# Optimization experiments

Hardware: AMD Instinct MI355X
Metric: run time of the kernel (lower is better)

The kernel has to match this reference:

```python
import jax, jax.numpy as jnp
import numpy as np

N, B, D, H, E = 1024, 8, 768, 8, 16384
DH = D // H
EPS = 1e-5


def setup_inputs() -> dict:
    key = jax.random.key(0)
    ks = jax.random.split(key, 12)
    s = 0.02
    return {
        "x": jax.random.normal(ks[0], (N, B, D), jnp.float32),
        "edge_index": jax.random.randint(ks[1], (B, 2, E), 0, N, jnp.int32),
        "gcn_W": jax.random.normal(ks[2], (D, D), jnp.float32) * s,
        "gcn_b": jnp.zeros((D,), jnp.float32),
        "in_proj_w": jax.random.normal(ks[3], (3 * D, D), jnp.float32) * s,
        "in_proj_b": jnp.zeros((3 * D,), jnp.float32),
        "out_proj_w": jax.random.normal(ks[4], (D, D), jnp.float32) * s,
        "out_proj_b": jnp.zeros((D,), jnp.float32),
        "gate_w": jax.random.normal(ks[5], (D, 2 * D), jnp.float32) * s,
        "gate_b": jnp.zeros((D,), jnp.float32),
        "ln_g": jnp.ones((D,), jnp.float32),
        "ln_b": jnp.zeros((D,), jnp.float32),
    }


def _gcn(xb, edge_index, gcn_W, gcn_b):
    # xb: [B, N, D] node features; edge_index: [B, 2, E]
    h = xb @ gcn_W.T  # linear first, as in PyG GCNConv
    loops = jnp.arange(N, dtype=edge_index.dtype)

    def agg(h_b, ei_b):
        src = jnp.concatenate([ei_b[0], loops])  # add self-loops
        dst = jnp.concatenate([ei_b[1], loops])
        deg = jax.ops.segment_sum(jnp.ones_like(src, h_b.dtype), dst, num_segments=N)
        dinv = jnp.where(deg > 0, jax.lax.rsqrt(deg), 0.0)
        norm = dinv[src] * dinv[dst]  # symmetric normalization
        msg = norm[:, None] * h_b[src]
        return jax.ops.segment_sum(msg, dst, num_segments=N)

    return jax.vmap(agg)(h, edge_index) + gcn_b  # [B, N, D]


def _mha(x, in_proj_w, in_proj_b, out_proj_w, out_proj_b):
    # x: [N, B, D] (seq-first, as nn.MultiheadAttention default)
    qkv = x @ in_proj_w.T + in_proj_b  # [N, B, 3D]
    q, k, v = jnp.split(qkv, 3, axis=-1)

    def heads(t):  # [N, B, D] -> [B, H, N, DH]
        return t.reshape(N, B, H, DH).transpose(1, 2, 0, 3)

    q, k, v = heads(q), heads(k), heads(v)
    scores = jnp.einsum("bhqd,bhkd->bhqk", q, k) / jnp.sqrt(jnp.float32(DH))
    attn = jax.nn.softmax(scores, axis=-1)
    ctx = jnp.einsum("bhqk,bhkd->bhqd", attn, v)  # [B, H, N, DH]
    ctx = ctx.transpose(2, 0, 1, 3).reshape(N, B, D)
    return ctx @ out_proj_w.T + out_proj_b


def _layernorm(x, g, b):
    mu = jnp.mean(x, axis=-1, keepdims=True)
    var = jnp.mean(jnp.square(x - mu), axis=-1, keepdims=True)
    return (x - mu) * jax.lax.rsqrt(var + EPS) * g + b


def reference(x, edge_index, gcn_W, gcn_b, in_proj_w, in_proj_b,
              out_proj_w, out_proj_b, gate_w, gate_b, ln_g, ln_b):
    xb = x.transpose(1, 0, 2)  # [B, N, D]
    gcn_out = _gcn(xb, edge_index, gcn_W, gcn_b).transpose(1, 0, 2)  # [N, B, D]
    attn_out = _mha(x, in_proj_w, in_proj_b, out_proj_w, out_proj_b)  # [N, B, D]
    combined = jnp.concatenate([gcn_out, attn_out], axis=-1)
    gate = jax.nn.sigmoid(combined @ gate_w.T + gate_b)
    fused = gate * gcn_out + (1.0 - gate) * attn_out
    return _layernorm(fused + x, ln_g, ln_b)
```

## Files before the change

### kernel.cpp

```cpp
#include <hip/hip_runtime.h>


typedef __attribute__((ext_vector_type(8))) short b16x8;
typedef __attribute__((ext_vector_type(4))) float f32x4;

using gu32 = __attribute__((address_space(1))) const unsigned int;
using lu32 = __attribute__((address_space(3))) unsigned int;

constexpr int N  = 1024;
constexpr int B  = 8;
constexpr int D  = 768;
constexpr int H  = 8;
constexpr int DH = 96;
constexpr int E  = 16384;
constexpr int M  = N * B;
constexpr float LN_EPS = 1e-5f;

#define DEV static __device__ __forceinline__
#define GLOAD(SRC, DST) __builtin_amdgcn_global_load_lds((gu32*)(SRC), (lu32*)(DST), 16, 0, 0)

DEV unsigned short f2b(float f) {
  unsigned u = __float_as_uint(f);
  u += 0x7fffu + ((u >> 16) & 1u);
  return (unsigned short)(u >> 16);
}
DEV float b2f(unsigned short h) { return __uint_as_float(((unsigned)h) << 16); }

constexpr int CS0 = 1572864;
constexpr int CS1 = CS0 + 147456;
constexpr int CS2 = CS1 + 442368;
constexpr int CS3 = CS2 + 147456;
constexpr int CS4 = CS3 + 294912;
__global__ void cast_all_kernel(
    const float* __restrict__ x, const float* __restrict__ gcnW,
    const float* __restrict__ ipw, const float* __restrict__ opw,
    const float* __restrict__ gw,
    unsigned short* __restrict__ xb16, unsigned short* __restrict__ wcat,
    unsigned short* __restrict__ wout, unsigned short* __restrict__ wgate) {
  const int i = blockIdx.x * 256 + threadIdx.x;
  if (i >= CS4) return;
  const float* in; unsigned short* out; int off;
  if (i < CS0)      { in = x;    out = xb16;           off = i; }
  else if (i < CS1) { in = gcnW; out = wcat;           off = i - CS0; }
  else if (i < CS2) { in = ipw;  out = wcat + 589824;  off = i - CS1; }
  else if (i < CS3) { in = opw;  out = wout;           off = i - CS2; }
  else              { in = gw;   out = wgate;          off = i - CS3; }
  float4 v = ((const float4*)in)[off];
  ushort4 o;
  o.x = f2b(v.x); o.y = f2b(v.y); o.z = f2b(v.z); o.w = f2b(v.w);
  ((ushort4*)out)[off] = o;
}

__global__ void zero_i32_kernel(int* __restrict__ p, int n) {
  int i = blockIdx.x * 256 + threadIdx.x;
  if (i < n) p[i] = 0;
}

__global__ void edge_count_kernel(const int* __restrict__ ei, int* __restrict__ cnt) {
  int i = blockIdx.x * 256 + threadIdx.x;
  int b = i >> 14, e = i & (E - 1);
  int dst = ei[(b << 15) + E + e];
  atomicAdd(&cnt[(b << 10) + dst], 1);
}

__global__ __launch_bounds__(1024) void scan_offs_kernel(
    const int* __restrict__ cnt, int* __restrict__ offs,
    int* __restrict__ cursor, float* __restrict__ dinv) {
  __shared__ int buf[1024];
  const int b = blockIdx.x, i = threadIdx.x, g = (b << 10) + i;
  const int c = cnt[g];
  buf[i] = c;
  __syncthreads();
  for (int off = 1; off < 1024; off <<= 1) {
    int t = (i >= off) ? buf[i - off] : 0;
    __syncthreads();
    buf[i] += t;
    __syncthreads();
  }
  const int excl = buf[i] - c;
  offs[g] = excl;
  cursor[g] = excl;
  dinv[g] = rsqrtf((float)(c + 1));
}

__global__ void edge_fill_kernel(const int* __restrict__ ei,
                                 int* __restrict__ cursor, int* __restrict__ elist) {
  int i = blockIdx.x * 256 + threadIdx.x;
  int b = i >> 14, e = i & (E - 1);
  int src = ei[(b << 15) + e];
  int dst = ei[(b << 15) + E + e];
  int slot = atomicAdd(&cursor[(b << 10) + dst], 1);
  elist[(b << 14) + slot] = src;
}

constexpr int EPI_FUSED = 0;
constexpr int EPI_ATTN  = 1;
constexpr int EPI_GATE  = 2;

template <int EPI, int BN, int K, int GX, int GY>
__global__ __launch_bounds__(256) void gemm_bt(
    const unsigned short* __restrict__ A, const unsigned short* __restrict__ W,
    const float* __restrict__ bias,
    void* __restrict__ p0, void* __restrict__ p1, void* __restrict__ p2,
    void* __restrict__ p3) {
  constexpr int NW = BN / 32;
  constexpr int NT = K / 32;
  __shared__ __align__(16) unsigned short sA[2][128][32];
  __shared__ __align__(16) unsigned short sB[2][BN][32];
  const int tid = threadIdx.x;
  const int lane = tid & 63, wid = tid >> 6;
  const int wm = wid >> 1, wn = wid & 1;
  const int bid = blockIdx.x;
  const int xcd = bid & 7, slot = bid >> 3;
  const int by = xcd * (GY / 8) + slot / GX;
  const int bx = slot % GX;
  const int m0 = by * 128, n0 = bx * BN;
  const int l15 = lane & 15, lhi = lane >> 4;
  const int srow = lane >> 2;
  const int scol = (((lane & 3) ^ ((lane >> 3) & 3))) * 8;
  const int rcol = ((lhi ^ ((l15 >> 1) & 3))) * 8;

  f32x4 acc[4][NW] = {};

  const unsigned short* pa = A + ((size_t)(m0 + wid * 32 + srow)) * K + scol;
  const unsigned short* pb = W + ((size_t)(n0 + wid * (BN / 4) + srow)) * K + scol;

  auto stage = [&](int buf) {
    GLOAD(pa,          &sA[buf][wid * 32][0]);
    GLOAD(pa + 16 * K, &sA[buf][wid * 32 + 16][0]);
    GLOAD(pb,          &sB[buf][wid * (BN / 4)][0]);
    if constexpr (BN == 128) GLOAD(pb + 16 * K, &sB[buf][wid * 32 + 16][0]);
    pa += 32; pb += 32;
  };

  stage(0);
  int cur = 0;
  for (int kt = 0; kt < NT; ++kt) {
    if (kt + 1 < NT) {
      stage(cur ^ 1);
      if constexpr (BN == 128) asm volatile("s_waitcnt vmcnt(4)" ::: "memory");
      else                     asm volatile("s_waitcnt vmcnt(3)" ::: "memory");
    } else {
      asm volatile("s_waitcnt vmcnt(0)" ::: "memory");
    }
    __builtin_amdgcn_s_barrier();
    __builtin_amdgcn_sched_barrier(0);

    b16x8 af[4], bfr[NW];
#pragma unroll
    for (int i = 0; i < 4; ++i)
      af[i] = *(const b16x8*)&sA[cur][wm * 64 + i * 16 + l15][rcol];
#pragma unroll
    for (int j = 0; j < NW; ++j)
      bfr[j] = *(const b16x8*)&sB[cur][wn * (BN / 2) + j * 16 + l15][rcol];
#pragma unroll
    for (int i = 0; i < 4; ++i)
#pragma unroll
      for (int j = 0; j < NW; ++j)
        acc[i][j] = __builtin_amdgcn_mfma_f32_16x16x32_bf16(af[i], bfr[j], acc[i][j], 0, 0, 0);

    __builtin_amdgcn_sched_barrier(0);
    __builtin_amdgcn_s_barrier();
    cur ^= 1;
  }

#pragma unroll
  for (int i = 0; i < 4; ++i) {
#pragma unroll
    for (int j = 0; j < NW; ++j) {
      const int c = n0 + wn * (BN / 2) + j * 16 + l15;
      float bv;
      if constexpr (EPI == EPI_FUSED) bv = (c < 768) ? 0.0f : bias[c - 768];
      else bv = bias[c];
#pragma unroll
      for (int g = 0; g < 4; ++g) {
        const int r = m0 + wm * 64 + i * 16 + lhi * 4 + g;
        float v = acc[i][j][g] + bv;
        if constexpr (EPI == EPI_FUSED) {
          const int n = r >> 3, b = r & 7;
          if (c < 768) {
            ((unsigned short*)p0)[((size_t)((b << 10) + n)) * 768 + c] = f2b(v);
          } else {
            const int cc2 = c - 768;
            const int sec = cc2 / 768, cc = cc2 - sec * 768;
            const int hd = cc / 96, dh = cc - hd * 96;
            unsigned short* dst =
                (sec == 0) ? (unsigned short*)p1
                           : (sec == 1 ? (unsigned short*)p2 : (unsigned short*)p3);
            size_t idx;
            if (sec < 2) idx = ((size_t)((b * 8 + hd) * 1024 + n)) * 96 + dh;
            else         idx = ((size_t)((b * 8 + hd) * 96 + dh)) * 1024 + n;
            dst[idx] = f2b(v);
          }
        } else if constexpr (EPI == EPI_ATTN) {
          ((unsigned short*)p0)[(size_t)r * 1536 + 768 + c] = f2b(v);
        } else {
          ((unsigned short*)p0)[(size_t)r * 768 + c] =
              f2b(1.0f / (1.0f + __expf(-v)));
        }
      }
    }
  }
}

__global__ __launch_bounds__(256) void attn_kernel(
    const unsigned short* __restrict__ qb, const unsigned short* __restrict__ kb,
    const unsigned short* __restrict__ vb, unsigned short* __restrict__ ctx) {
  __shared__ __align__(16) unsigned short sK[64][104];
  __shared__ __align__(16) unsigned short sV[96][72];
  __shared__ __align__(16) unsigned short sP[4][16][72];
  const int tid = threadIdx.x, lane = tid & 63, wid = tid >> 6;
  const int l15 = lane & 15, lhi = lane >> 4;
  const int bid = blockIdx.x;
  const int xcd = bid & 7, slot = bid >> 3;
  const int bh = xcd * 8 + (slot >> 4);
  const int q0 = (slot & 15) * 64;
  const float SCL = 0.14724445f;

  b16x8 qf[3];
  const size_t qbase = ((size_t)bh * 1024 + q0 + wid * 16 + l15) * 96 + lhi * 8;
#pragma unroll
  for (int ks = 0; ks < 3; ++ks) qf[ks] = *(const b16x8*)(qb + qbase + ks * 32);

  const int c0 = tid, c1 = 256 + tid, c2 = 512 + tid;
  const unsigned short* kp0 = kb + ((size_t)bh * 1024 + c0 / 12) * 96 + (c0 % 12) * 8;
  const unsigned short* kp1 = kb + ((size_t)bh * 1024 + c1 / 12) * 96 + (c1 % 12) * 8;
  const unsigned short* kp2 = kb + ((size_t)bh * 1024 + c2 / 12) * 96 + (c2 % 12) * 8;
  const unsigned short* vp0 = vb + ((size_t)bh * 96 + (c0 >> 3)) * 1024 + (c0 & 7) * 8;
  const unsigned short* vp1 = vb + ((size_t)bh * 96 + (c1 >> 3)) * 1024 + (c1 & 7) * 8;
  const unsigned short* vp2 = vb + ((size_t)bh * 96 + (c2 >> 3)) * 1024 + (c2 & 7) * 8;
  unsigned short* sk0 = &sK[c0 / 12][(c0 % 12) * 8];
  unsigned short* sk1 = &sK[c1 / 12][(c1 % 12) * 8];
  unsigned short* sk2 = &sK[c2 / 12][(c2 % 12) * 8];
  unsigned short* sv0 = &sV[c0 >> 3][(c0 & 7) * 8];
  unsigned short* sv1 = &sV[c1 >> 3][(c1 & 7) * 8];
  unsigned short* sv2 = &sV[c2 >> 3][(c2 & 7) * 8];

  uint4 k0 = *(const uint4*)kp0, k1 = *(const uint4*)kp1, k2 = *(const uint4*)kp2;
  uint4 v0 = *(const uint4*)vp0, v1 = *(const uint4*)vp1, v2 = *(const uint4*)vp2;

  f32x4 accO[6] = {};
  float ssum[4] = {0.f, 0.f, 0.f, 0.f};

  for (int kt = 0; kt < 16; ++kt) {
    __syncthreads();
    *(uint4*)sk0 = k0; *(uint4*)sk1 = k1; *(uint4*)sk2 = k2;
    *(uint4*)sv0 = v0; *(uint4*)sv1 = v1; *(uint4*)sv2 = v2;
    __syncthreads();
    if (kt < 15) {
      kp0 += 64 * 96; kp1 += 64 * 96; kp2 += 64 * 96;
      vp0 += 64;      vp1 += 64;      vp2 += 64;
      k0 = *(const uint4*)kp0; k1 = *(const uint4*)kp1; k2 = *(const uint4*)kp2;
      v0 = *(const uint4*)vp0; v1 = *(const uint4*)vp1; v2 = *(const uint4*)vp2;
    }

    f32x4 sf[4] = {};
    __builtin_amdgcn_s_setprio(1);
#pragma unroll
    for (int f = 0; f < 4; ++f) {
#pragma unroll
      for (int ks = 0; ks < 3; ++ks) {
        b16x8 kf = *(const b16x8*)&sK[f * 16 + l15][ks * 32 + lhi * 8];
        sf[f] = __builtin_amdgcn_mfma_f32_16x16x32_bf16(qf[ks], kf, sf[f], 0, 0, 0);
      }
    }
    __builtin_amdgcn_s_setprio(0);

#pragma unroll
    for (int g = 0; g < 4; ++g) {
#pragma unroll
      for (int f = 0; f < 4; ++f) {
        const float pv = exp2f(sf[f][g] * SCL);
        sP[wid][lhi * 4 + g][f * 16 + l15] = f2b(pv);
        ssum[g] += pv;
      }
    }

    __builtin_amdgcn_s_setprio(1);
#pragma unroll
    for (int ks = 0; ks < 2; ++ks) {
      b16x8 pa = *(const b16x8*)&sP[wid][l15][ks * 32 + lhi * 8];
#pragma unroll
      for (int o = 0; o < 6; ++o) {
        b16x8 vf = *(const b16x8*)&sV[o * 16 + l15][ks * 32 + lhi * 8];
        accO[o] = __builtin_amdgcn_mfma_f32_16x16x32_bf16(pa, vf, accO[o], 0, 0, 0);
      }
    }
    __builtin_amdgcn_s_setprio(0);
  }

#pragma unroll
  for (int g = 0; g < 4; ++g) {
#pragma unroll
    for (int msk = 1; msk < 16; msk <<= 1) ssum[g] += __shfl_xor(ssum[g], msk);
  }

  const int b = bh >> 3, hd = bh & 7;
  float rinv[4];
#pragma unroll
  for (int g = 0; g < 4; ++g) rinv[g] = 1.0f / ssum[g];
#pragma unroll
  for (int o = 0; o < 6; ++o)
#pragma unroll
    for (int g = 0; g < 4; ++g) {
      const int qrow = q0 + wid * 16 + lhi * 4 + g;
      ctx[((size_t)qrow * 8 + b) * 768 + hd * 96 + o * 16 + l15] =
          f2b(accO[o][g] * rinv[g]);
    }
}

__global__ __launch_bounds__(192) void gcn_agg_kernel(
    const unsigned short* __restrict__ h16,
    const int* __restrict__ cnt, const int* __restrict__ offs,
    const int* __restrict__ elist, const float* __restrict__ dinv,
    const float* __restrict__ gcn_b, unsigned short* __restrict__ cat16) {
  const int bn = blockIdx.x;
  const int b = bn >> 10, n = bn & 1023;
  const int d = threadIdx.x * 4;
  const float dn = dinv[bn];
  const size_t hrow = (size_t)bn * 768;
  ushort4 hv = *(const ushort4*)(h16 + hrow + d);
  float a0 = dn * dn * b2f(hv.x), a1 = dn * dn * b2f(hv.y);
  float a2 = dn * dn * b2f(hv.z), a3 = dn * dn * b2f(hv.w);
  const int st = offs[bn], cv = cnt[bn];
  const int* ep = elist + (b << 14) + st;
  int i = 0;
  for (; i + 2 <= cv; i += 2) {
    const int s0 = ep[i], s1 = ep[i + 1];
    const float nv0 = dinv[(b << 10) + s0] * dn;
    const float nv1 = dinv[(b << 10) + s1] * dn;
    const ushort4 r0 = *(const ushort4*)(h16 + ((size_t)((b << 10) + s0)) * 768 + d);
    const ushort4 r1 = *(const ushort4*)(h16 + ((size_t)((b << 10) + s1)) * 768 + d);
    a0 += nv0 * b2f(r0.x) + nv1 * b2f(r1.x);
    a1 += nv0 * b2f(r0.y) + nv1 * b2f(r1.y);
    a2 += nv0 * b2f(r0.z) + nv1 * b2f(r1.z);
    a3 += nv0 * b2f(r0.w) + nv1 * b2f(r1.w);
  }
  if (i < cv) {
    const int s0 = ep[i];
    const float nv0 = dinv[(b << 10) + s0] * dn;
    const ushort4 r0 = *(const ushort4*)(h16 + ((size_t)((b << 10) + s0)) * 768 + d);
    a0 += nv0 * b2f(r0.x); a1 += nv0 * b2f(r0.y);
    a2 += nv0 * b2f(r0.z); a3 += nv0 * b2f(r0.w);
  }
  const float4 bb = *(const float4*)(gcn_b + d);
  a0 += bb.x; a1 += bb.y; a2 += bb.z; a3 += bb.w;
  const size_t crow = ((size_t)n * 8 + b) * 1536;
  ushort4 co; co.x = f2b(a0); co.y = f2b(a1); co.z = f2b(a2); co.w = f2b(a3);
  *(ushort4*)(cat16 + crow + d) = co;
}

__global__ __launch_bounds__(192) void ln_fuse_kernel(
    const unsigned short* __restrict__ gate16,
    const unsigned short* __restrict__ cat16,
    const float* __restrict__ x,
    const float* __restrict__ lng, const float* __restrict__ lnb,
    float* __restrict__ out) {
  const int r = blockIdx.x;
  const int t = threadIdx.x, lane = t & 63, wid = t >> 6;
  const int d = t * 4;
  const size_t xrow = (size_t)r * 768;
  const size_t crow = (size_t)r * 1536;
  const ushort4 gv = *(const ushort4*)(gate16 + xrow + d);
  const ushort4 cv = *(const ushort4*)(cat16 + crow + d);
  const ushort4 av = *(const ushort4*)(cat16 + crow + 768 + d);
  const float4 xv = *(const float4*)(x + xrow + d);
  const float g0 = b2f(gv.x), g1 = b2f(gv.y), g2 = b2f(gv.z), g3 = b2f(gv.w);
  float f0 = g0 * b2f(cv.x) + (1.f - g0) * b2f(av.x) + xv.x;
  float f1 = g1 * b2f(cv.y) + (1.f - g1) * b2f(av.y) + xv.y;
  float f2 = g2 * b2f(cv.z) + (1.f - g2) * b2f(av.z) + xv.z;
  float f3 = g3 * b2f(cv.w) + (1.f - g3) * b2f(av.w) + xv.w;
  float s1 = f0 + f1 + f2 + f3;
  float s2 = f0 * f0 + f1 * f1 + f2 * f2 + f3 * f3;
#pragma unroll
  for (int msk = 1; msk < 64; msk <<= 1) {
    s1 += __shfl_xor(s1, msk);
    s2 += __shfl_xor(s2, msk);
  }
  __shared__ float p1[3], p2[3];
  if (lane == 0) { p1[wid] = s1; p2[wid] = s2; }
  __syncthreads();
  s1 = p1[0] + p1[1] + p1[2];
  s2 = p2[0] + p2[1] + p2[2];
  const float mu = s1 * (1.f / 768.f);
  float var = s2 * (1.f / 768.f) - mu * mu;
  var = fmaxf(var, 0.f);
  const float rstd = rsqrtf(var + LN_EPS);
  const float4 lg = *(const float4*)(lng + d);
  const float4 lb = *(const float4*)(lnb + d);
  float4 o;
  o.x = (f0 - mu) * rstd * lg.x + lb.x;
  o.y = (f1 - mu) * rstd * lg.y + lb.y;
  o.z = (f2 - mu) * rstd * lg.z + lb.z;
  o.w = (f3 - mu) * rstd * lg.w + lb.w;
  *(float4*)(out + xrow + d) = o;
}

extern "C" void kernel_launch(void* const* d_in, const int* in_sizes, int n_in,
                              void* d_out, int out_size, void* d_ws, size_t ws_size,
                              hipStream_t stream) {
  const float* x     = (const float*)d_in[0];
  const int*   ei    = (const int*)d_in[1];
  const float* gcnW  = (const float*)d_in[2];
  const float* gcnb  = (const float*)d_in[3];
  const float* ipw   = (const float*)d_in[4];
  const float* ipb   = (const float*)d_in[5];
  const float* opw   = (const float*)d_in[6];
  const float* opb   = (const float*)d_in[7];
  const float* gw    = (const float*)d_in[8];
  const float* gb    = (const float*)d_in[9];
  const float* lng   = (const float*)d_in[10];
  const float* lnb   = (const float*)d_in[11];
  float* out = (float*)d_out;

  char* p = (char*)d_ws;
  auto alloc = [&](size_t bytes) { void* q = p; p += (bytes + 255) & ~(size_t)255; return q; };

  unsigned short* xb16  = (unsigned short*)alloc((size_t)M * 768 * 2);
  unsigned short* wcat  = (unsigned short*)alloc((size_t)3072 * 768 * 2);
  unsigned short* wout  = (unsigned short*)alloc((size_t)768 * 768 * 2);
  unsigned short* wgate = (unsigned short*)alloc((size_t)768 * 1536 * 2);
  unsigned short* qb    = (unsigned short*)alloc((size_t)B * H * N * DH * 2);
  unsigned short* kb    = (unsigned short*)alloc((size_t)B * H * N * DH * 2);
  unsigned short* vb    = (unsigned short*)alloc((size_t)B * H * DH * N * 2);
  unsigned short* h16   = (unsigned short*)alloc((size_t)M * 768 * 2);
  unsigned short* cat16 = (unsigned short*)alloc((size_t)M * 1536 * 2);
  int* cnt    = (int*)alloc(8192 * 4);
  int* offs   = (int*)alloc(8192 * 4);
  int* cursor = (int*)alloc(8192 * 4);
  float* dinv = (float*)alloc(8192 * 4);
  int* elist  = (int*)alloc((size_t)B * E * 4);

  unsigned short* ctx16  = xb16;
  unsigned short* gate16 = qb;

  cast_all_kernel<<<(CS4 + 255) / 256, 256, 0, stream>>>(
      x, gcnW, ipw, opw, gw, xb16, wcat, wout, wgate);

  zero_i32_kernel<<<32, 256, 0, stream>>>(cnt, 8192);
  edge_count_kernel<<<(B * E) / 256, 256, 0, stream>>>(ei, cnt);
  scan_offs_kernel<<<8, 1024, 0, stream>>>(cnt, offs, cursor, dinv);
  edge_fill_kernel<<<(B * E) / 256, 256, 0, stream>>>(ei, cursor, elist);

  gemm_bt<EPI_FUSED, 128, 768, 24, 64><<<1536, 256, 0, stream>>>(
      xb16, wcat, ipb, (void*)h16, (void*)qb, (void*)kb, (void*)vb);
  attn_kernel<<<1024, 256, 0, stream>>>(qb, kb, vb, ctx16);
  gcn_agg_kernel<<<8192, 192, 0, stream>>>(h16, cnt, offs, elist, dinv, gcnb, cat16);
  gemm_bt<EPI_ATTN, 64, 768, 12, 64><<<768, 256, 0, stream>>>(
      ctx16, wout, opb, (void*)cat16, nullptr, nullptr, nullptr);
  gemm_bt<EPI_GATE, 64, 1536, 12, 64><<<768, 256, 0, stream>>>(
      cat16, wgate, gb, (void*)gate16, nullptr, nullptr, nullptr);

  ln_fuse_kernel<<<8192, 192, 0, stream>>>(gate16, cat16, x, lng, lnb, out);
}
```

Measured before the change: 257.5 us.

## Merge cast with edge counting and attention with GCN aggregation into single launches

Folds the bf16 cast and the edge-degree counting into one launch split by block index, replaces the zero kernel with a memset, and merges the attention kernel with the GCN aggregation kernel so both independent workloads run in one grid. The goal is to cut launch overhead and let the two independent tasks overlap on the GPU, filling idle CUs. The aggregation blocks now launch with 256 threads but use only 192, and they reserve the attention kernel's shared memory, which may lower occupancy for that part.

```diff
diff --git a/kernel.cpp b/kernel.cpp
--- a/kernel.cpp
+++ b/kernel.cpp
@@ -31,36 +31,34 @@
 constexpr int CS2 = CS1 + 442368;
 constexpr int CS3 = CS2 + 147456;
 constexpr int CS4 = CS3 + 294912;
-__global__ void cast_all_kernel(
+constexpr int CAST_BLOCKS = CS4 / 256;
+constexpr int CNT_BLOCKS  = (B * E) / 256;
+__global__ void cast_count_kernel(
     const float* __restrict__ x, const float* __restrict__ gcnW,
     const float* __restrict__ ipw, const float* __restrict__ opw,
     const float* __restrict__ gw,
     unsigned short* __restrict__ xb16, unsigned short* __restrict__ wcat,
-    unsigned short* __restrict__ wout, unsigned short* __restrict__ wgate) {
-  const int i = blockIdx.x * 256 + threadIdx.x;
-  if (i >= CS4) return;
-  const float* in; unsigned short* out; int off;
-  if (i < CS0)      { in = x;    out = xb16;           off = i; }
-  else if (i < CS1) { in = gcnW; out = wcat;           off = i - CS0; }
-  else if (i < CS2) { in = ipw;  out = wcat + 589824;  off = i - CS1; }
-  else if (i < CS3) { in = opw;  out = wout;           off = i - CS2; }
-  else              { in = gw;   out = wgate;          off = i - CS3; }
-  float4 v = ((const float4*)in)[off];
-  ushort4 o;
-  o.x = f2b(v.x); o.y = f2b(v.y); o.z = f2b(v.z); o.w = f2b(v.w);
-  ((ushort4*)out)[off] = o;
-}
-
-__global__ void zero_i32_kernel(int* __restrict__ p, int n) {
-  int i = blockIdx.x * 256 + threadIdx.x;
-  if (i < n) p[i] = 0;
-}
-
-__global__ void edge_count_kernel(const int* __restrict__ ei, int* __restrict__ cnt) {
-  int i = blockIdx.x * 256 + threadIdx.x;
-  int b = i >> 14, e = i & (E - 1);
-  int dst = ei[(b << 15) + E + e];
-  atomicAdd(&cnt[(b << 10) + dst], 1);
+    unsigned short* __restrict__ wout, unsigned short* __restrict__ wgate,
+    const int* __restrict__ ei, int* __restrict__ cnt) {
+  const int blk = blockIdx.x;
+  if (blk < CAST_BLOCKS) {
+    const int i = blk * 256 + threadIdx.x;
+    const float* in; unsigned short* out; int off;
+    if (i < CS0)      { in = x;    out = xb16;           off = i; }
+    else if (i < CS1) { in = gcnW; out = wcat;           off = i - CS0; }
+    else if (i < CS2) { in = ipw;  out = wcat + 589824;  off = i - CS1; }
+    else if (i < CS3) { in = opw;  out = wout;           off = i - CS2; }
+    else              { in = gw;   out = wgate;          off = i - CS3; }
+    float4 v = ((const float4*)in)[off];
+    ushort4 o;
+    o.x = f2b(v.x); o.y = f2b(v.y); o.z = f2b(v.z); o.w = f2b(v.w);
+    ((ushort4*)out)[off] = o;
+  } else {
+    const int j = (blk - CAST_BLOCKS) * 256 + threadIdx.x;
+    const int b = j >> 14, e = j & (E - 1);
+    const int dst = ei[(b << 15) + E + e];
+    atomicAdd(&cnt[(b << 10) + dst], 1);
+  }
 }
 
 __global__ __launch_bounds__(1024) void scan_offs_kernel(
@@ -203,12 +201,57 @@
   }
 }
 
-__global__ __launch_bounds__(256) void attn_kernel(
+__global__ __launch_bounds__(256) void attn_agg_kernel(
     const unsigned short* __restrict__ qb, const unsigned short* __restrict__ kb,
-    const unsigned short* __restrict__ vb, unsigned short* __restrict__ ctx) {
+    const unsigned short* __restrict__ vb, unsigned short* __restrict__ ctx,
+    const unsigned short* __restrict__ h16,
+    const int* __restrict__ cnt, const int* __restrict__ offs,
+    const int* __restrict__ elist, const float* __restrict__ dinv,
+    const float* __restrict__ gcn_b, unsigned short* __restrict__ cat16) {
   __shared__ __align__(16) unsigned short sK[64][104];
   __shared__ __align__(16) unsigned short sV[96][72];
   __shared__ __align__(16) unsigned short sP[4][16][72];
+
+  if (blockIdx.x >= 1024) {
+    if (threadIdx.x >= 192) return;
+    const int abid = blockIdx.x - 1024;
+    const int b = abid & 7, n = abid >> 3;
+    const int bn = (b << 10) + n;
+    const int d = threadIdx.x * 4;
+    const float dn = dinv[bn];
+    const size_t hrow = (size_t)bn * 768;
+    ushort4 hv = *(const ushort4*)(h16 + hrow + d);
+    float a0 = dn * dn * b2f(hv.x), a1 = dn * dn * b2f(hv.y);
+    float a2 = dn * dn * b2f(hv.z), a3 = dn * dn * b2f(hv.w);
+    const int st = offs[bn], cv = cnt[bn];
+    const int* ep = elist + (b << 14) + st;
+    int i = 0;
+    for (; i + 2 <= cv; i += 2) {
+      const int s0 = ep[i], s1 = ep[i + 1];
+      const float nv0 = dinv[(b << 10) + s0] * dn;
+      const float nv1 = dinv[(b << 10) + s1] * dn;
+      const ushort4 r0 = *(const ushort4*)(h16 + ((size_t)((b << 10) + s0)) * 768 + d);
+      const ushort4 r1 = *(const ushort4*)(h16 + ((size_t)((b << 10) + s1)) * 768 + d);
+      a0 += nv0 * b2f(r0.x) + nv1 * b2f(r1.x);
+      a1 += nv0 * b2f(r0.y) + nv1 * b2f(r1.y);
+      a2 += nv0 * b2f(r0.z) + nv1 * b2f(r1.z);
+      a3 += nv0 * b2f(r0.w) + nv1 * b2f(r1.w);
+    }
+    if (i < cv) {
+      const int s0 = ep[i];
+      const float nv0 = dinv[(b << 10) + s0] * dn;
+      const ushort4 r0 = *(const ushort4*)(h16 + ((size_t)((b << 10) + s0)) * 768 + d);
+      a0 += nv0 * b2f(r0.x); a1 += nv0 * b2f(r0.y);
+      a2 += nv0 * b2f(r0.z); a3 += nv0 * b2f(r0.w);
+    }
+    const float4 bb = *(const float4*)(gcn_b + d);
+    a0 += bb.x; a1 += bb.y; a2 += bb.z; a3 += bb.w;
+    const size_t crow = ((size_t)n * 8 + b) * 1536;
+    ushort4 co; co.x = f2b(a0); co.y = f2b(a1); co.z = f2b(a2); co.w = f2b(a3);
+    *(ushort4*)(cat16 + crow + d) = co;
+    return;
+  }
+
   const int tid = threadIdx.x, lane = tid & 63, wid = tid >> 6;
   const int l15 = lane & 15, lhi = lane >> 4;
   const int bid = blockIdx.x;
@@ -307,47 +350,6 @@
       ctx[((size_t)qrow * 8 + b) * 768 + hd * 96 + o * 16 + l15] =
           f2b(accO[o][g] * rinv[g]);
     }
-}
-
-__global__ __launch_bounds__(192) void gcn_agg_kernel(
-    const unsigned short* __restrict__ h16,
-    const int* __restrict__ cnt, const int* __restrict__ offs,
-    const int* __restrict__ elist, const float* __restrict__ dinv,
-    const float* __restrict__ gcn_b, unsigned short* __restrict__ cat16) {
-  const int bn = blockIdx.x;
-  const int b = bn >> 10, n = bn & 1023;
-  const int d = threadIdx.x * 4;
-  const float dn = dinv[bn];
-  const size_t hrow = (size_t)bn * 768;
-  ushort4 hv = *(const ushort4*)(h16 + hrow + d);
-  float a0 = dn * dn * b2f(hv.x), a1 = dn * dn * b2f(hv.y);
-  float a2 = dn * dn * b2f(hv.z), a3 = dn * dn * b2f(hv.w);
-  const int st = offs[bn], cv = cnt[bn];
-  const int* ep = elist + (b << 14) + st;
-  int i = 0;
-  for (; i + 2 <= cv; i += 2) {
-    const int s0 = ep[i], s1 = ep[i + 1];
-    const float nv0 = dinv[(b << 10) + s0] * dn;
-    const float nv1 = dinv[(b << 10) + s1] * dn;
-    const ushort4 r0 = *(const ushort4*)(h16 + ((size_t)((b << 10) + s0)) * 768 + d);
-    const ushort4 r1 = *(const ushort4*)(h16 + ((size_t)((b << 10) + s1)) * 768 + d);
-    a0 += nv0 * b2f(r0.x) + nv1 * b2f(r1.x);
-    a1 += nv0 * b2f(r0.y) + nv1 * b2f(r1.y);
-    a2 += nv0 * b2f(r0.z) + nv1 * b2f(r1.z);
-    a3 += nv0 * b2f(r0.w) + nv1 * b2f(r1.w);
-  }
-  if (i < cv) {
-    const int s0 = ep[i];
-    const float nv0 = dinv[(b << 10) + s0] * dn;
-    const ushort4 r0 = *(const ushort4*)(h16 + ((size_t)((b << 10) + s0)) * 768 + d);
-    a0 += nv0 * b2f(r0.x); a1 += nv0 * b2f(r0.y);
-    a2 += nv0 * b2f(r0.z); a3 += nv0 * b2f(r0.w);
-  }
-  const float4 bb = *(const float4*)(gcn_b + d);
-  a0 += bb.x; a1 += bb.y; a2 += bb.z; a3 += bb.w;
-  const size_t crow = ((size_t)n * 8 + b) * 1536;
-  ushort4 co; co.x = f2b(a0); co.y = f2b(a1); co.z = f2b(a2); co.w = f2b(a3);
-  *(ushort4*)(cat16 + crow + d) = co;
 }
 
 __global__ __launch_bounds__(192) void ln_fuse_kernel(
@@ -434,18 +436,17 @@
   unsigned short* ctx16  = xb16;
   unsigned short* gate16 = qb;
 
-  cast_all_kernel<<<(CS4 + 255) / 256, 256, 0, stream>>>(
-      x, gcnW, ipw, opw, gw, xb16, wcat, wout, wgate);
-
-  zero_i32_kernel<<<32, 256, 0, stream>>>(cnt, 8192);
-  edge_count_kernel<<<(B * E) / 256, 256, 0, stream>>>(ei, cnt);
+  hipMemsetAsync(cnt, 0, 8192 * 4, stream);
+  cast_count_kernel<<<CAST_BLOCKS + CNT_BLOCKS, 256, 0, stream>>>(
+      x, gcnW, ipw, opw, gw, xb16, wcat, wout, wgate, ei, cnt);
+
   scan_offs_kernel<<<8, 1024, 0, stream>>>(cnt, offs, cursor, dinv);
   edge_fill_kernel<<<(B * E) / 256, 256, 0, stream>>>(ei, cursor, elist);
 
   gemm_bt<EPI_FUSED, 128, 768, 24, 64><<<1536, 256, 0, stream>>>(
       xb16, wcat, ipb, (void*)h16, (void*)qb, (void*)kb, (void*)vb);
-  attn_kernel<<<1024, 256, 0, stream>>>(qb, kb, vb, ctx16);
-  gcn_agg_kernel<<<8192, 192, 0, stream>>>(h16, cnt, offs, elist, dinv, gcnb, cat16);
+  attn_agg_kernel<<<1024 + 8192, 256, 0, stream>>>(
+      qb, kb, vb, ctx16, h16, cnt, offs, elist, dinv, gcnb, cat16);
   gemm_bt<EPI_ATTN, 64, 768, 12, 64><<<768, 256, 0, stream>>>(
       ctx16, wout, opb, (void*)cat16, nullptr, nullptr, nullptr);
   gemm_bt<EPI_GATE, 64, 1536, 12, 64><<<768, 256, 0, stream>>>(
```

Result: no change. 256.6 us (median of 2 runs) (-0.3%).
